# Optimization experiments

Hardware: AMD Instinct MI355X
Metric: run time of the kernel (lower is better)

The kernel has to match this reference:

```python
import jax, jax.numpy as jnp
import numpy as np

K = 3           # kernel_size
PAD = 1         # padding
HEADS = 6
C = 192
CH = C // HEADS           # channels per head = 32
SCALE = CH ** (-0.5)
KK = K * K                # 9


def unfold3(x):
    # x: [N,C,H,W] -> [N,C,9,H,W] (im2col with k=3, pad=1, stride=1)
    N, c, H, W = x.shape
    xp = jnp.pad(x, ((0, 0), (0, 0), (PAD, PAD), (PAD, PAD)))
    return jnp.stack([xp[:, :, i:i + H, j:j + W] for i in range(K) for j in range(K)], axis=2)


def fold3(y):
    # y: [N,C,9,H,W] -> [N,C,H,W] (scatter-add inverse of unfold3)
    N, c, kk, H, W = y.shape
    out = jnp.zeros((N, c, H + 2 * PAD, W + 2 * PAD), dtype=y.dtype)
    idx = 0
    for i in range(K):
        for j in range(K):
            out = out.at[:, :, i:i + H, j:j + W].add(y[:, :, idx])
            idx += 1
    return out[:, :, PAD:PAD + H, PAD:PAD + W]


def setup_inputs() -> dict:
    key = jax.random.key(0)
    ks = jax.random.split(key, 6)
    N, H, W = 16, 56, 56
    s = 0.02
    return {
        "x": jax.random.normal(ks[0], (N, C, H, W), jnp.float32),
        "Wv": jax.random.normal(ks[1], (C, C), jnp.float32) * s,          # fc (no bias)
        "Wa": jax.random.normal(ks[2], (C, KK * KK * HEADS), jnp.float32) * s,  # fc_att weight
        "ba": jax.random.normal(ks[3], (KK * KK * HEADS,), jnp.float32) * s,
        "Wp": jax.random.normal(ks[4], (C, C), jnp.float32) * s,          # fc_proj weight
        "bp": jax.random.normal(ks[5], (C,), jnp.float32) * s,
    }


def reference(x, Wv, Wa, ba, Wp, bp):
    N, c, H, W = x.shape
    HW = H * W
    # value projection (pointwise linear over channels)
    v = jnp.einsum("nchw,cd->ndhw", x, Wv)
    # unfold values: [N,C,9,H,W] -> [N,heads,ch,9,HW] -> [N,heads,HW,9,ch]
    vu = unfold3(v).reshape(N, HEADS, CH, KK, HW).transpose(0, 1, 4, 3, 2)
    # attention logits from (avg-pooled, here identity since stride=1) input
    att = jnp.einsum("nchw,ck->nhwk", x, Wa) + ba       # [N,H,W,81*heads]
    att = att.reshape(N, HW, HEADS, KK, KK).transpose(0, 2, 1, 3, 4)  # [N,heads,HW,9,9]
    att = jax.nn.softmax(att * SCALE, axis=-1)          # dropout is identity at inference
    # apply per-position 9x9 attention to the 9 gathered neighbors
    out = jnp.einsum("nhpkl,nhplc->nhpkc", att, vu)      # [N,heads,HW,9,ch]
    # fold back: layout (heads, ch, kk) matches unfold layout (C, kk)
    out = out.transpose(0, 1, 4, 3, 2).reshape(N, c, KK, H, W)
    folded = fold3(out)                                  # [N,C,H,W]
    # output projection
    return jnp.einsum("nchw,cd->ndhw", folded, Wp) + bp[None, :, None, None]
```

## Files before the change

kernel.cpp:

```cpp
#include <hip/hip_runtime.h>
#include <hip/hip_bf16.h>
#include <math.h>

#define HW 3136
#define NC 192
#define NHEADS 6
#define IMG 56
#define NATT 486
#define YSTR 768
#define ATT_SCALE 0.17677669529663687f

typedef __attribute__((ext_vector_type(8))) short short8;
typedef __attribute__((ext_vector_type(8))) unsigned short ushort8;
typedef __attribute__((ext_vector_type(4))) float float4v;

__device__ __forceinline__ float bf2f(unsigned short u) {
    unsigned int x = ((unsigned int)u) << 16;
    return __builtin_bit_cast(float, x);
}
__device__ __forceinline__ unsigned short f2bf(float f) {
    __hip_bfloat16 h = __float2bfloat16(f);
    return __builtin_bit_cast(unsigned short, h);
}
__device__ __forceinline__ void gload_lds16(const void* g, void* l) {
    __builtin_amdgcn_global_load_lds((const __attribute__((address_space(1))) void*)g,
                                     (__attribute__((address_space(3))) void*)l, 16, 0, 0);
}

__global__ __launch_bounds__(256) void transpose_x(const float* __restrict__ x,
                                                   unsigned short* __restrict__ xt)
{
    __shared__ float tile[64][65];
    int bx = blockIdx.x;
    int n = (bx * 64) / HW;
    int hw0 = (bx * 64) % HW;
    int c0 = blockIdx.y * 64;
    int tl = threadIdx.x & 63, tg = threadIdx.x >> 6;
    const float* xn = x + (size_t)n * NC * HW;
#pragma unroll
    for (int i = 0; i < 16; ++i)
        tile[tg * 16 + i][tl] = xn[(size_t)(c0 + tg * 16 + i) * HW + hw0 + tl];
    __syncthreads();
    unsigned short* xp = xt + ((size_t)n * HW + hw0) * NC + c0;
#pragma unroll
    for (int i = 0; i < 16; ++i) {
        int hwr = tg * 16 + i;
        xp[(size_t)hwr * NC + tl] = f2bf(tile[tl][hwr]);
    }
}

__global__ __launch_bounds__(256) void prep_weights(
    const float* __restrict__ Wv, const float* __restrict__ Wa, const float* __restrict__ Wp,
    const float* __restrict__ ba,
    unsigned short* __restrict__ Wall, unsigned short* __restrict__ Wpt,
    float* __restrict__ ball)
{
    int idx = blockIdx.x * 256 + threadIdx.x;
    if (idx < 36864) {
        int d = idx / 192, k = idx - d * 192;
        Wpt[idx] = f2bf(Wp[(size_t)k * NC + d]);
    }
    if (idx < 147456) {
        int d = idx / 192, k = idx - d * 192;
        unsigned short val;
        float bv = 0.f;
        if (d < 192) {
            val = f2bf(Wv[(size_t)k * NC + d]);
        } else {
            int dp = d - 192;
            int head = dp / 96, rr = dp - head * 96;
            int k9 = rr / 10, l = rr - k9 * 10;
            bool valid = (k9 < 9) && (l < 9);
            int src = head * 81 + k9 * 9 + l;
            val = valid ? f2bf(Wa[(size_t)k * NATT + src]) : (unsigned short)0;
            bv = valid ? ba[src] : 0.f;
        }
        Wall[idx] = val;
        if (k == 0) ball[d] = bv;
    }
}

__global__ __launch_bounds__(256) void gemm_big(
    const unsigned short* __restrict__ A, const unsigned short* __restrict__ W,
    const float* __restrict__ ball, unsigned short* __restrict__ Y)
{
    __shared__ __align__(16) unsigned short As[2][4096];
    __shared__ __align__(16) unsigned short Bs[2][4096];
    int t = threadIdx.x, lane = t & 63, wave = t >> 6;
    int col0 = blockIdx.x * 128, row0 = blockIdx.y * 128;
    int fr = lane & 15, fq = lane >> 4;
    int wm = (wave >> 1) * 64, wn = (wave & 1) * 64;
    int srow = lane >> 2;
    int soff = (lane & 3) * 16;
    const char* Ab = (const char*)A;
    const char* Wb = (const char*)W;

    float4v acc[4][4] = {};

#define STAGE_BIG(buf, k0)                                                        \
    {                                                                             \
        _Pragma("unroll")                                                         \
        for (int i = 0; i < 2; ++i) {                                             \
            int j = wave * 2 + i;                                                 \
            gload_lds16(Ab + (size_t)(row0 + j * 16 + srow) * 384 + (k0)*2 + soff,\
                        (char*)As[buf] + j * 1024);                               \
            gload_lds16(Wb + (size_t)(col0 + j * 16 + srow) * 384 + (k0)*2 + soff,\
                        (char*)Bs[buf] + j * 1024);                               \
        }                                                                         \
    }

    STAGE_BIG(0, 0);
    for (int s = 0; s < 6; ++s) {
        if (s < 5) STAGE_BIG((s + 1) & 1, (s + 1) * 32);
        __syncthreads();
        int buf = s & 1;
        short8 af[4], bf[4];
#pragma unroll
        for (int mi = 0; mi < 4; ++mi)
            af[mi] = *(const short8*)((const char*)As[buf] + (wm + mi * 16 + fr) * 64 + fq * 16);
#pragma unroll
        for (int ni = 0; ni < 4; ++ni)
            bf[ni] = *(const short8*)((const char*)Bs[buf] + (wn + ni * 16 + fr) * 64 + fq * 16);
#pragma unroll
        for (int mi = 0; mi < 4; ++mi)
#pragma unroll
            for (int ni = 0; ni < 4; ++ni)
                acc[mi][ni] = __builtin_amdgcn_mfma_f32_16x16x32_bf16(
                    af[mi], bf[ni], acc[mi][ni], 0, 0, 0);
        __syncthreads();
    }

#pragma unroll
    for (int ni = 0; ni < 4; ++ni) {
        int col = col0 + wn + ni * 16 + fr;
        float b = ball[col];
#pragma unroll
        for (int mi = 0; mi < 4; ++mi) {
            int row = row0 + wm + mi * 16 + fq * 4;
#pragma unroll
            for (int r = 0; r < 4; ++r)
                Y[(size_t)(row + r) * YSTR + col] = f2bf(acc[mi][ni][r] + b);
        }
    }
#undef STAGE_BIG
}

__global__ __launch_bounds__(256) void gemm_small(
    const unsigned short* __restrict__ A,
    const unsigned short* __restrict__ B,
    const float* __restrict__ bias, float* __restrict__ out)
{
    __shared__ __align__(16) unsigned short As[2][2048];
    __shared__ __align__(16) unsigned short Bs[2][8192];
    int t = threadIdx.x, lane = t & 63, wave = t >> 6;
    int n0 = blockIdx.x * 256, m0 = blockIdx.y * 64;
    int fr = lane & 15, fq = lane >> 4;
    int srow = lane >> 2, soff = (lane & 3) * 16;
    const char* Ab = (const char*)A;
    const char* Bb = (const char*)B;

    float4v acc[4][4] = {};

#define STAGE_SMALL(buf, k0)                                                      \
    {                                                                             \
        gload_lds16(Ab + (size_t)(m0 + wave * 16 + srow) * 384 + (k0)*2 + soff,   \
                    (char*)As[buf] + wave * 1024);                                \
        _Pragma("unroll")                                                         \
        for (int i = 0; i < 4; ++i) {                                             \
            int j = wave * 4 + i;                                                 \
            gload_lds16(Bb + (size_t)(n0 + j * 16 + srow) * 384 + (k0)*2 + soff,  \
                        (char*)Bs[buf] + j * 1024);                               \
        }                                                                         \
    }

    STAGE_SMALL(0, 0);
    for (int s = 0; s < 6; ++s) {
        if (s < 5) STAGE_SMALL((s + 1) & 1, (s + 1) * 32);
        __syncthreads();
        int buf = s & 1;
        short8 af[4], bf[4];
#pragma unroll
        for (int mi = 0; mi < 4; ++mi)
            af[mi] = *(const short8*)((const char*)As[buf] + (mi * 16 + fr) * 64 + fq * 16);
#pragma unroll
        for (int ni = 0; ni < 4; ++ni)
            bf[ni] = *(const short8*)((const char*)Bs[buf] + (wave * 64 + ni * 16 + fr) * 64 + fq * 16);
#pragma unroll
        for (int mi = 0; mi < 4; ++mi)
#pragma unroll
            for (int ni = 0; ni < 4; ++ni)
                acc[mi][ni] = __builtin_amdgcn_mfma_f32_16x16x32_bf16(
                    af[mi], bf[ni], acc[mi][ni], 0, 0, 0);
        __syncthreads();
    }

#pragma unroll
    for (int ni = 0; ni < 4; ++ni) {
        int n = n0 + wave * 64 + ni * 16 + fr;
        int img = n / HW, phw = n - img * HW;
        float* op = out + (size_t)img * (NC * HW) + phw;
#pragma unroll
        for (int mi = 0; mi < 4; ++mi) {
            int m = m0 + mi * 16 + fq * 4;
#pragma unroll
            for (int r = 0; r < 4; ++r)
                op[(size_t)(m + r) * HW] = acc[mi][ni][r] + bias[m + r];
        }
    }
#undef STAGE_SMALL
}

__global__ __launch_bounds__(256) void fused_att_agg(
    const unsigned short* __restrict__ Y, unsigned short* __restrict__ fold)
{
    __shared__ __align__(16) unsigned short vt[12 * 32 * 32];
    __shared__ float swc[224 * 25];
    int t = threadIdx.x;
    int bid = blockIdx.x;
    int head = bid % NHEADS; int tmp = bid / NHEADS;
    int tcol = tmp & 1; tmp >>= 1;
    int trow = tmp % 7; int img = tmp / 7;
    int h0 = trow * 8, w0 = tcol * 28;

    {
        const unsigned short* Yv = Y + head * 32;
#pragma unroll
        for (int i = 0; i < 6; ++i) {
            int u = i * 256 + t;
            int slot = u >> 2, q = u & 3;
            int vrow = slot >> 5, vcol = slot & 31;
            int hh = h0 - 2 + vrow, ww = w0 - 2 + vcol;
            bool ok = (hh >= 0) & (hh < IMG) & (ww >= 0) & (ww < IMG);
            ushort8 val = {};
            if (ok)
                val = *(const ushort8*)(Yv + (size_t)(img * HW + hh * IMG + ww) * YSTR + q * 8);
            *(ushort8*)&vt[(size_t)slot * 32 + q * 8] = val;
        }
    }

    if (t < 224) {
        int ph = t / 28, pw = t - (t / 28) * 28;
        int h = h0 + ph, w = w0 + pw;
        const unsigned short* attn =
            Y + (size_t)(img * HW + h * IMG + w) * YSTR + 192 + head * 96;
        float wc[25];
#pragma unroll
        for (int d = 0; d < 25; ++d) wc[d] = 0.f;
#pragma unroll
        for (int k = 0; k < 9; ++k) {
            const int oky = k / 3 - 1, okx = k % 3 - 1;
            int hh = h - oky, ww = w - okx;
            if (hh < 0 || hh >= IMG || ww < 0 || ww >= IMG) continue;
            const unsigned short* ap = attn - (ptrdiff_t)(oky * IMG + okx) * YSTR + k * 10;
            ushort8 a8;
            __builtin_memcpy(&a8, ap, 16);
            float a[9];
#pragma unroll
            for (int l = 0; l < 8; ++l) a[l] = bf2f(a8[l]);
            a[8] = bf2f(ap[8]);
            float m = -1e30f;
#pragma unroll
            for (int l = 0; l < 9; ++l) m = fmaxf(m, a[l]);
            float s = 0.f;
#pragma unroll
            for (int l = 0; l < 9; ++l) {
                a[l] = __expf((a[l] - m) * ATT_SCALE);
                s += a[l];
            }
            float r = 1.f / s;
#pragma unroll
            for (int l = 0; l < 9; ++l) {
                const int dy = (l / 3 - 1) - oky + 2;
                const int dx = (l % 3 - 1) - okx + 2;
                wc[dy * 5 + dx] += a[l] * r;
            }
        }
        float* o = swc + t * 25;
#pragma unroll
        for (int d = 0; d < 25; ++d) o[d] = wc[d];
    }
    __syncthreads();

#pragma unroll
    for (int i = 0; i < 4; ++i) {
        int item = i * 256 + t;
        if (item < 896) {
            int p = item >> 2, q8 = item & 3;
            int ph = p / 28, pw = p - (p / 28) * 28;
            const float* wp = swc + p * 25;
            float acc[8];
#pragma unroll
            for (int j = 0; j < 8; ++j) acc[j] = 0.f;
#pragma unroll
            for (int d = 0; d < 25; ++d) {
                const int dy = d / 5, dx = d % 5;
                float wf = wp[d];
                ushort8 vv = *(const ushort8*)&vt[(((ph + dy) << 5) + (pw + dx)) * 32 + q8 * 8];
#pragma unroll
                for (int j = 0; j < 8; ++j)
                    acc[j] += wf * bf2f(vv[j]);
            }
            int rem = img * HW + (h0 + ph) * IMG + (w0 + pw);
            unsigned short* fo = fold + (size_t)rem * NC + head * 32 + q8 * 8;
            ushort8 ov;
#pragma unroll
            for (int j = 0; j < 8; ++j) ov[j] = f2bf(acc[j]);
            *(ushort8*)fo = ov;
        }
    }
}

extern "C" void kernel_launch(void* const* d_in, const int* in_sizes, int n_in,
                              void* d_out, int out_size, void* d_ws, size_t ws_size,
                              hipStream_t stream)
{
    const float* x  = (const float*)d_in[0];
    const float* Wv = (const float*)d_in[1];
    const float* Wa = (const float*)d_in[2];
    const float* ba = (const float*)d_in[3];
    const float* Wp = (const float*)d_in[4];
    const float* bp = (const float*)d_in[5];
    float* out = (float*)d_out;

    unsigned short* xt    = (unsigned short*)d_ws;
    unsigned short* Y     = xt + 9633792;
    unsigned short* Wall  = Y + 38535168;
    unsigned short* Wpt   = Wall + 147456;
    float*          ball  = (float*)(Wpt + 36864);
    unsigned short* foldb = xt;

    dim3 blk(256);
    prep_weights<<<576, blk, 0, stream>>>(Wv, Wa, Wp, ba, Wall, Wpt, ball);
    transpose_x<<<dim3(784, 3), blk, 0, stream>>>(x, xt);
    gemm_big<<<dim3(6, 392), blk, 0, stream>>>(xt, Wall, ball, Y);
    fused_att_agg<<<1344, blk, 0, stream>>>(Y, foldb);
    gemm_small<<<dim3(196, 3), blk, 0, stream>>>(Wpt, foldb, bp, out);
}
```

Before: 196.8 us.

## Keep softmax weights in registers and overlap value loads with attention compute

Restructures the fused attention-aggregation kernel so the 25 combined weights stay in registers and each thread computes all 32 channels for its own pixel, which removes the shared-memory weight buffer. Value-tile global loads are issued into registers before the softmax work and written to LDS only afterwards, so their latency overlaps the attention computation. It also uses clamped, branch-free addressing for the halo and attention loads, a channel-quarter-planar LDS layout, and launch bounds requesting 4 blocks per SM. The cost is higher register pressure from holding the staged values and weights, and 32 of the 256 threads sit idle during aggregation.

```diff
diff --git a/kernel.cpp b/kernel.cpp
--- a/kernel.cpp
+++ b/kernel.cpp
@@ -210,11 +210,10 @@
 #undef STAGE_SMALL
 }
 
-__global__ __launch_bounds__(256) void fused_att_agg(
+__global__ __launch_bounds__(256, 4) void fused_att_agg(
     const unsigned short* __restrict__ Y, unsigned short* __restrict__ fold)
 {
-    __shared__ __align__(16) unsigned short vt[12 * 32 * 32];
-    __shared__ float swc[224 * 25];
+    __shared__ __align__(16) char vt[25600];
     int t = threadIdx.x;
     int bid = blockIdx.x;
     int head = bid % NHEADS; int tmp = bid / NHEADS;
@@ -222,36 +221,38 @@
     int trow = tmp % 7; int img = tmp / 7;
     int h0 = trow * 8, w0 = tcol * 28;
 
-    {
-        const unsigned short* Yv = Y + head * 32;
-#pragma unroll
-        for (int i = 0; i < 6; ++i) {
-            int u = i * 256 + t;
-            int slot = u >> 2, q = u & 3;
-            int vrow = slot >> 5, vcol = slot & 31;
-            int hh = h0 - 2 + vrow, ww = w0 - 2 + vcol;
-            bool ok = (hh >= 0) & (hh < IMG) & (ww >= 0) & (ww < IMG);
-            ushort8 val = {};
-            if (ok)
-                val = *(const ushort8*)(Yv + (size_t)(img * HW + hh * IMG + ww) * YSTR + q * 8);
-            *(ushort8*)&vt[(size_t)slot * 32 + q * 8] = val;
-        }
-    }
-
+    const unsigned short* Yv = Y + head * 32;
+    ushort8 stg[6];
+#pragma unroll
+    for (int i = 0; i < 6; ++i) {
+        int u = i * 256 + t;
+        int slot = u >> 2, q = u & 3;
+        int vrow = slot >> 5, vcol = slot & 31;
+        int hh = h0 - 2 + vrow, ww = w0 - 2 + vcol;
+        bool ok = (hh >= 0) & (hh < IMG) & (ww >= 0) & (ww < IMG);
+        int hc = min(max(hh, 0), IMG - 1);
+        int wcl = min(max(ww, 0), IMG - 1);
+        ushort8 val = *(const ushort8*)(Yv + (size_t)(img * HW + hc * IMG + wcl) * YSTR + q * 8);
+        if (!ok) val = (ushort8){};
+        stg[i] = val;
+    }
+
+    int ph = t / 28, pw = t - (t / 28) * 28;
+    int h = h0 + ph, w = w0 + pw;
+    float wc[25];
+#pragma unroll
+    for (int d = 0; d < 25; ++d) wc[d] = 0.f;
     if (t < 224) {
-        int ph = t / 28, pw = t - (t / 28) * 28;
-        int h = h0 + ph, w = w0 + pw;
-        const unsigned short* attn =
-            Y + (size_t)(img * HW + h * IMG + w) * YSTR + 192 + head * 96;
-        float wc[25];
-#pragma unroll
-        for (int d = 0; d < 25; ++d) wc[d] = 0.f;
+        const unsigned short* Yatt = Y + 192 + head * 96;
 #pragma unroll
         for (int k = 0; k < 9; ++k) {
             const int oky = k / 3 - 1, okx = k % 3 - 1;
             int hh = h - oky, ww = w - okx;
-            if (hh < 0 || hh >= IMG || ww < 0 || ww >= IMG) continue;
-            const unsigned short* ap = attn - (ptrdiff_t)(oky * IMG + okx) * YSTR + k * 10;
+            bool ok = (hh >= 0) & (hh < IMG) & (ww >= 0) & (ww < IMG);
+            int hc = min(max(hh, 0), IMG - 1);
+            int wcl = min(max(ww, 0), IMG - 1);
+            const unsigned short* ap =
+                Yatt + (size_t)(img * HW + hc * IMG + wcl) * YSTR + k * 10;
             ushort8 a8;
             __builtin_memcpy(&a8, ap, 16);
             float a[9];
@@ -267,45 +268,47 @@
                 a[l] = __expf((a[l] - m) * ATT_SCALE);
                 s += a[l];
             }
-            float r = 1.f / s;
+            float g = ok ? (1.f / s) : 0.f;
 #pragma unroll
             for (int l = 0; l < 9; ++l) {
                 const int dy = (l / 3 - 1) - oky + 2;
                 const int dx = (l % 3 - 1) - okx + 2;
-                wc[dy * 5 + dx] += a[l] * r;
+                wc[dy * 5 + dx] += a[l] * g;
             }
         }
-        float* o = swc + t * 25;
-#pragma unroll
-        for (int d = 0; d < 25; ++d) o[d] = wc[d];
+    }
+
+#pragma unroll
+    for (int i = 0; i < 6; ++i) {
+        int u = i * 256 + t;
+        int slot = u >> 2, q = u & 3;
+        *(ushort8*)(vt + q * 6400 + slot * 16) = stg[i];
     }
     __syncthreads();
 
-#pragma unroll
-    for (int i = 0; i < 4; ++i) {
-        int item = i * 256 + t;
-        if (item < 896) {
-            int p = item >> 2, q8 = item & 3;
-            int ph = p / 28, pw = p - (p / 28) * 28;
-            const float* wp = swc + p * 25;
+    if (t < 224) {
+        int base = (ph * 32 + pw) * 16;
+        int pos = img * HW + h * IMG + w;
+        unsigned short* fo = fold + (size_t)pos * NC + head * 32;
+#pragma unroll
+        for (int q = 0; q < 4; ++q) {
+            const char* vq = vt + q * 6400 + base;
             float acc[8];
 #pragma unroll
             for (int j = 0; j < 8; ++j) acc[j] = 0.f;
 #pragma unroll
             for (int d = 0; d < 25; ++d) {
                 const int dy = d / 5, dx = d % 5;
-                float wf = wp[d];
-                ushort8 vv = *(const ushort8*)&vt[(((ph + dy) << 5) + (pw + dx)) * 32 + q8 * 8];
+                float wf = wc[d];
+                ushort8 vv = *(const ushort8*)(vq + dy * 512 + dx * 16);
 #pragma unroll
                 for (int j = 0; j < 8; ++j)
                     acc[j] += wf * bf2f(vv[j]);
             }
-            int rem = img * HW + (h0 + ph) * IMG + (w0 + pw);
-            unsigned short* fo = fold + (size_t)rem * NC + head * 32 + q8 * 8;
             ushort8 ov;
 #pragma unroll
             for (int j = 0; j < 8; ++j) ov[j] = f2bf(acc[j]);
-            *(ushort8*)fo = ov;
+            *(ushort8*)(fo + q * 8) = ov;
         }
     }
 }
```

Result: no change. 195.2 us (-0.8%).
